# Kernel tuning notes

Hardware: AMD Instinct MI355X
Metric: run time of the kernel (lower is better)

Reference implementation:

```python
import jax, jax.numpy as jnp
import numpy as np

N = 32
R = 128  # num_regions
F = 128  # num_features


def setup_inputs() -> dict:
    key = jax.random.key(0)
    k1, k2, k3, k4 = jax.random.split(key, 4)
    x1 = jax.random.normal(k1, (N, R * F), dtype=jnp.float32)
    x2 = jax.random.normal(k2, (N, R * F), dtype=jnp.float32)
    sigma = jax.random.normal(k3, (1,), dtype=jnp.float32) * 100.0
    mean = jax.random.normal(k4, (1,), dtype=jnp.float32)
    return {"x1": x1, "x2": x2, "sigma": sigma, "mean": mean}


def reference(x1, x2, sigma, mean):
    # (N, R, 1, F) - (N, 1, R, F) - mean -> (N, R, R, F)
    a = x1.reshape(N, R, 1, F)
    b = x2.reshape(N, 1, R, F)
    diff = a - b - mean  # mean is shape (1,), broadcasts over F
    distance_squared = jnp.sum(diff * diff, axis=-1)  # (N, R, R)
    kernel_value = jnp.exp(-distance_squared / (2.0 * sigma[0] ** 2))
    return jax.nn.softmax(kernel_value, axis=-1)
```

## Files before the change

### kernel.cpp

```cpp
#include <hip/hip_runtime.h>

#define NB 32
#define RR 128
#define FF 128
#define SB 132

__global__ __launch_bounds__(256) void gauss_fused(const float* __restrict__ x1,
                                                   const float* __restrict__ x2,
                                                   const float* __restrict__ sigma,
                                                   const float* __restrict__ mean,
                                                   float* __restrict__ out) {
  __shared__ __align__(16) float sh_b[FF * SB];
  __shared__ __align__(16) float sh_a[16 * FF];

  const int d = blockIdx.x;
  const int xcd = d & 7;
  const int k = d >> 3;
  const int n = (xcd << 2) + (k >> 3);
  const int i0 = (k & 7) << 4;
  const int tid = threadIdx.x;
  const int tx = tid & 31;
  const int ty = tid >> 5;

  const float mval = mean[0];
  const float sg = sigma[0];
  const float cneg = -1.0f / (2.0f * sg * sg);

  const float* __restrict__ x2base = x2 + (size_t)n * RR * FF;
  const int jj = tid >> 3;
  const int fo = (tid & 7) << 2;

  float4 q0, q1, q2, q3, q4, q5, q6, q7, q8, q9, q10, q11, q12, q13, q14, q15;
#define LDQ(fc, p) *(const float4*)(x2base + (size_t)(jj + ((p) << 5)) * FF + ((fc) << 5) + fo)
  q0 = LDQ(0, 0);  q1 = LDQ(0, 1);  q2 = LDQ(0, 2);  q3 = LDQ(0, 3);
  q4 = LDQ(1, 0);  q5 = LDQ(1, 1);  q6 = LDQ(1, 2);  q7 = LDQ(1, 3);
  q8 = LDQ(2, 0);  q9 = LDQ(2, 1);  q10 = LDQ(2, 2); q11 = LDQ(2, 3);
  q12 = LDQ(3, 0); q13 = LDQ(3, 1); q14 = LDQ(3, 2); q15 = LDQ(3, 3);
#undef LDQ
  const float4* asrc = (const float4*)(x1 + (size_t)(n * RR + i0) * FF);
  const float4 v0 = asrc[tid];
  const float4 v1 = asrc[tid + 256];

  ((float4*)sh_a)[tid] = make_float4(v0.x - mval, v0.y - mval, v0.z - mval, v0.w - mval);
  ((float4*)sh_a)[tid + 256] = make_float4(v1.x - mval, v1.y - mval, v1.z - mval, v1.w - mval);
#define STW(q, fc, p)                                    \
  {                                                      \
    const int f0 = ((fc) << 5) + fo;                     \
    const int j = jj + ((p) << 5);                       \
    sh_b[(f0 + 0) * SB + j] = (q).x;                     \
    sh_b[(f0 + 1) * SB + j] = (q).y;                     \
    sh_b[(f0 + 2) * SB + j] = (q).z;                     \
    sh_b[(f0 + 3) * SB + j] = (q).w;                     \
  }
  STW(q0, 0, 0)  STW(q1, 0, 1)  STW(q2, 0, 2)  STW(q3, 0, 3)
  STW(q4, 1, 0)  STW(q5, 1, 1)  STW(q6, 1, 2)  STW(q7, 1, 3)
  STW(q8, 2, 0)  STW(q9, 2, 1)  STW(q10, 2, 2) STW(q11, 2, 3)
  STW(q12, 3, 0) STW(q13, 3, 1) STW(q14, 3, 2) STW(q15, 3, 3)
#undef STW
  __syncthreads();

  float acc00 = 0.f, acc01 = 0.f, acc02 = 0.f, acc03 = 0.f;
  float acc10 = 0.f, acc11 = 0.f, acc12 = 0.f, acc13 = 0.f;
  const int j0 = tx << 2;
  const float* __restrict__ arow0 = sh_a + ty * FF;
  const float* __restrict__ arow1 = sh_a + (ty + 8) * FF;

#pragma unroll 4
  for (int fq = 0; fq < 32; ++fq) {
    const float4 a0 = *(const float4*)(arow0 + (fq << 2));
    const float4 a1 = *(const float4*)(arow1 + (fq << 2));
#pragma unroll
    for (int c = 0; c < 4; ++c) {
      const float4 b = *(const float4*)(sh_b + ((fq << 2) + c) * SB + j0);
      const float a0c = (c == 0) ? a0.x : (c == 1) ? a0.y : (c == 2) ? a0.z : a0.w;
      const float a1c = (c == 0) ? a1.x : (c == 1) ? a1.y : (c == 2) ? a1.z : a1.w;
      float d;
      d = a0c - b.x; acc00 = fmaf(d, d, acc00);
      d = a0c - b.y; acc01 = fmaf(d, d, acc01);
      d = a0c - b.z; acc02 = fmaf(d, d, acc02);
      d = a0c - b.w; acc03 = fmaf(d, d, acc03);
      d = a1c - b.x; acc10 = fmaf(d, d, acc10);
      d = a1c - b.y; acc11 = fmaf(d, d, acc11);
      d = a1c - b.z; acc12 = fmaf(d, d, acc12);
      d = a1c - b.w; acc13 = fmaf(d, d, acc13);
    }
  }

  const float k00 = __expf(acc00 * cneg);
  const float k01 = __expf(acc01 * cneg);
  const float k02 = __expf(acc02 * cneg);
  const float k03 = __expf(acc03 * cneg);
  const float k10 = __expf(acc10 * cneg);
  const float k11 = __expf(acc11 * cneg);
  const float k12 = __expf(acc12 * cneg);
  const float k13 = __expf(acc13 * cneg);

  float mx0 = fmaxf(fmaxf(k00, k01), fmaxf(k02, k03));
  float mx1 = fmaxf(fmaxf(k10, k11), fmaxf(k12, k13));
#pragma unroll
  for (int off = 16; off >= 1; off >>= 1) {
    mx0 = fmaxf(mx0, __shfl_xor(mx0, off, 64));
    mx1 = fmaxf(mx1, __shfl_xor(mx1, off, 64));
  }
  const float e00 = __expf(k00 - mx0);
  const float e01 = __expf(k01 - mx0);
  const float e02 = __expf(k02 - mx0);
  const float e03 = __expf(k03 - mx0);
  const float e10 = __expf(k10 - mx1);
  const float e11 = __expf(k11 - mx1);
  const float e12 = __expf(k12 - mx1);
  const float e13 = __expf(k13 - mx1);
  float s0 = e00 + e01 + e02 + e03;
  float s1 = e10 + e11 + e12 + e13;
#pragma unroll
  for (int off = 16; off >= 1; off >>= 1) {
    s0 += __shfl_xor(s0, off, 64);
    s1 += __shfl_xor(s1, off, 64);
  }
  const float r0 = 1.0f / s0;
  const float r1 = 1.0f / s1;

  *(float4*)(out + (size_t)(n * RR + i0 + ty) * RR + j0) =
      make_float4(e00 * r0, e01 * r0, e02 * r0, e03 * r0);
  *(float4*)(out + (size_t)(n * RR + i0 + ty + 8) * RR + j0) =
      make_float4(e10 * r1, e11 * r1, e12 * r1, e13 * r1);
}

extern "C" void kernel_launch(void* const* d_in, const int* in_sizes, int n_in,
                              void* d_out, int out_size, void* d_ws, size_t ws_size,
                              hipStream_t stream) {
  const float* x1 = (const float*)d_in[0];
  const float* x2 = (const float*)d_in[1];
  const float* sigma = (const float*)d_in[2];
  const float* mean = (const float*)d_in[3];
  float* out = (float*)d_out;
  (void)d_ws; (void)ws_size;

  gauss_fused<<<dim3(NB * 8), dim3(256), 0, stream>>>(x1, x2, sigma, mean, out);
}
```

Before: 65.59 us.

## Split feature dimension into two halves and overlap second-half load with first-half compute

The x2 tile is now staged in two feature halves with separate shared buffers. Global loads for the second half are issued before computing on the first half, so their latency is hidden behind the distance accumulation. The cost is an extra barrier and more live registers while the first half is computed. Total shared memory use stays about the same.

After: 65.70 us. No clear change (+0.2%).

```diff
diff --git a/kernel.cpp b/kernel.cpp
--- a/kernel.cpp
+++ b/kernel.cpp
@@ -3,6 +3,7 @@
 #define NB 32
 #define RR 128
 #define FF 128
+#define FT 64
 #define SB 132
 
 __global__ __launch_bounds__(256) void gauss_fused(const float* __restrict__ x1,
@@ -10,7 +11,7 @@
                                                    const float* __restrict__ sigma,
                                                    const float* __restrict__ mean,
                                                    float* __restrict__ out) {
-  __shared__ __align__(16) float sh_b[FF * SB];
+  __shared__ __align__(16) float sh_b[2][FT * SB];
   __shared__ __align__(16) float sh_a[16 * FF];
 
   const int d = blockIdx.x;
@@ -30,34 +31,18 @@
   const int jj = tid >> 3;
   const int fo = (tid & 7) << 2;
 
-  float4 q0, q1, q2, q3, q4, q5, q6, q7, q8, q9, q10, q11, q12, q13, q14, q15;
-#define LDQ(fc, p) *(const float4*)(x2base + (size_t)(jj + ((p) << 5)) * FF + ((fc) << 5) + fo)
-  q0 = LDQ(0, 0);  q1 = LDQ(0, 1);  q2 = LDQ(0, 2);  q3 = LDQ(0, 3);
-  q4 = LDQ(1, 0);  q5 = LDQ(1, 1);  q6 = LDQ(1, 2);  q7 = LDQ(1, 3);
-  q8 = LDQ(2, 0);  q9 = LDQ(2, 1);  q10 = LDQ(2, 2); q11 = LDQ(2, 3);
-  q12 = LDQ(3, 0); q13 = LDQ(3, 1); q14 = LDQ(3, 2); q15 = LDQ(3, 3);
-#undef LDQ
-  const float4* asrc = (const float4*)(x1 + (size_t)(n * RR + i0) * FF);
-  const float4 v0 = asrc[tid];
-  const float4 v1 = asrc[tid + 256];
-
-  ((float4*)sh_a)[tid] = make_float4(v0.x - mval, v0.y - mval, v0.z - mval, v0.w - mval);
-  ((float4*)sh_a)[tid + 256] = make_float4(v1.x - mval, v1.y - mval, v1.z - mval, v1.w - mval);
-#define STW(q, fc, p)                                    \
-  {                                                      \
-    const int f0 = ((fc) << 5) + fo;                     \
-    const int j = jj + ((p) << 5);                       \
-    sh_b[(f0 + 0) * SB + j] = (q).x;                     \
-    sh_b[(f0 + 1) * SB + j] = (q).y;                     \
-    sh_b[(f0 + 2) * SB + j] = (q).z;                     \
-    sh_b[(f0 + 3) * SB + j] = (q).w;                     \
+#define LDQ(t, fc, p) \
+  *(const float4*)(x2base + (size_t)(jj + ((p) << 5)) * FF + (t) * FT + ((fc) << 5) + fo)
+#define STW(q, t, fc, p)                              \
+  {                                                   \
+    const int f0 = ((fc) << 5) + fo;                  \
+    const int j = jj + ((p) << 5);                    \
+    float* dstp = sh_b[t];                            \
+    dstp[(f0 + 0) * SB + j] = (q).x;                  \
+    dstp[(f0 + 1) * SB + j] = (q).y;                  \
+    dstp[(f0 + 2) * SB + j] = (q).z;                  \
+    dstp[(f0 + 3) * SB + j] = (q).w;                  \
   }
-  STW(q0, 0, 0)  STW(q1, 0, 1)  STW(q2, 0, 2)  STW(q3, 0, 3)
-  STW(q4, 1, 0)  STW(q5, 1, 1)  STW(q6, 1, 2)  STW(q7, 1, 3)
-  STW(q8, 2, 0)  STW(q9, 2, 1)  STW(q10, 2, 2) STW(q11, 2, 3)
-  STW(q12, 3, 0) STW(q13, 3, 1) STW(q14, 3, 2) STW(q15, 3, 3)
-#undef STW
-  __syncthreads();
 
   float acc00 = 0.f, acc01 = 0.f, acc02 = 0.f, acc03 = 0.f;
   float acc10 = 0.f, acc11 = 0.f, acc12 = 0.f, acc13 = 0.f;
@@ -65,26 +50,57 @@
   const float* __restrict__ arow0 = sh_a + ty * FF;
   const float* __restrict__ arow1 = sh_a + (ty + 8) * FF;
 
-#pragma unroll 4
-  for (int fq = 0; fq < 32; ++fq) {
-    const float4 a0 = *(const float4*)(arow0 + (fq << 2));
-    const float4 a1 = *(const float4*)(arow1 + (fq << 2));
-#pragma unroll
-    for (int c = 0; c < 4; ++c) {
-      const float4 b = *(const float4*)(sh_b + ((fq << 2) + c) * SB + j0);
-      const float a0c = (c == 0) ? a0.x : (c == 1) ? a0.y : (c == 2) ? a0.z : a0.w;
-      const float a1c = (c == 0) ? a1.x : (c == 1) ? a1.y : (c == 2) ? a1.z : a1.w;
-      float d;
-      d = a0c - b.x; acc00 = fmaf(d, d, acc00);
-      d = a0c - b.y; acc01 = fmaf(d, d, acc01);
-      d = a0c - b.z; acc02 = fmaf(d, d, acc02);
-      d = a0c - b.w; acc03 = fmaf(d, d, acc03);
-      d = a1c - b.x; acc10 = fmaf(d, d, acc10);
-      d = a1c - b.y; acc11 = fmaf(d, d, acc11);
-      d = a1c - b.z; acc12 = fmaf(d, d, acc12);
-      d = a1c - b.w; acc13 = fmaf(d, d, acc13);
-    }
+#define COMPUTE_HALF(t)                                                          \
+  {                                                                              \
+    const float* __restrict__ bb = sh_b[t];                                      \
+    _Pragma("unroll 4") for (int fq = 0; fq < 16; ++fq) {                        \
+      const float4 a0 = *(const float4*)(arow0 + (t) * FT + (fq << 2));          \
+      const float4 a1 = *(const float4*)(arow1 + (t) * FT + (fq << 2));          \
+      _Pragma("unroll") for (int c = 0; c < 4; ++c) {                            \
+        const float4 b = *(const float4*)(bb + ((fq << 2) + c) * SB + j0);       \
+        const float a0c = (c == 0) ? a0.x : (c == 1) ? a0.y : (c == 2) ? a0.z : a0.w; \
+        const float a1c = (c == 0) ? a1.x : (c == 1) ? a1.y : (c == 2) ? a1.z : a1.w; \
+        float dd;                                                                \
+        dd = a0c - b.x; acc00 = fmaf(dd, dd, acc00);                             \
+        dd = a0c - b.y; acc01 = fmaf(dd, dd, acc01);                             \
+        dd = a0c - b.z; acc02 = fmaf(dd, dd, acc02);                             \
+        dd = a0c - b.w; acc03 = fmaf(dd, dd, acc03);                             \
+        dd = a1c - b.x; acc10 = fmaf(dd, dd, acc10);                             \
+        dd = a1c - b.y; acc11 = fmaf(dd, dd, acc11);                             \
+        dd = a1c - b.z; acc12 = fmaf(dd, dd, acc12);                             \
+        dd = a1c - b.w; acc13 = fmaf(dd, dd, acc13);                             \
+      }                                                                          \
+    }                                                                            \
   }
+
+  {
+    float4 q0 = LDQ(0, 0, 0), q1 = LDQ(0, 0, 1), q2 = LDQ(0, 0, 2), q3 = LDQ(0, 0, 3);
+    float4 q4 = LDQ(0, 1, 0), q5 = LDQ(0, 1, 1), q6 = LDQ(0, 1, 2), q7 = LDQ(0, 1, 3);
+    const float4* asrc = (const float4*)(x1 + (size_t)(n * RR + i0) * FF);
+    const float4 v0 = asrc[tid];
+    const float4 v1 = asrc[tid + 256];
+    ((float4*)sh_a)[tid] = make_float4(v0.x - mval, v0.y - mval, v0.z - mval, v0.w - mval);
+    ((float4*)sh_a)[tid + 256] = make_float4(v1.x - mval, v1.y - mval, v1.z - mval, v1.w - mval);
+    STW(q0, 0, 0, 0) STW(q1, 0, 0, 1) STW(q2, 0, 0, 2) STW(q3, 0, 0, 3)
+    STW(q4, 0, 1, 0) STW(q5, 0, 1, 1) STW(q6, 0, 1, 2) STW(q7, 0, 1, 3)
+  }
+  __syncthreads();
+
+  {
+    float4 q0 = LDQ(1, 0, 0), q1 = LDQ(1, 0, 1), q2 = LDQ(1, 0, 2), q3 = LDQ(1, 0, 3);
+    float4 q4 = LDQ(1, 1, 0), q5 = LDQ(1, 1, 1), q6 = LDQ(1, 1, 2), q7 = LDQ(1, 1, 3);
+
+    COMPUTE_HALF(0)
+
+    STW(q0, 1, 0, 0) STW(q1, 1, 0, 1) STW(q2, 1, 0, 2) STW(q3, 1, 0, 3)
+    STW(q4, 1, 1, 0) STW(q5, 1, 1, 1) STW(q6, 1, 1, 2) STW(q7, 1, 1, 3)
+  }
+  __syncthreads();
+
+  COMPUTE_HALF(1)
+#undef LDQ
+#undef STW
+#undef COMPUTE_HALF
 
   const float k00 = __expf(acc00 * cneg);
   const float k01 = __expf(acc01 * cneg);
```
